# Kernel optimization log

Hardware: AMD Instinct MI355X
Metric: run time of the kernel (lower is better)

## Reference

```python
import jax, jax.numpy as jnp
import numpy as np

N = 100000        # nodes
E = 1600000       # directed edges (avg degree 16)
EMB = 32          # emb_hidden_dim
HID = 16          # hidden
Q = 0.25          # magnetic charge
NUM_SYMP = 15
BY = 4            # num_birthyear_disc


def _norm(edge_index, edge_weight):
    # Magnetic Laplacian, 'sym' normalization, lambda_max=2:
    # L_hat(u,v) = -deg^{-1/2}(u) * A_sym(u,v) * deg^{-1/2}(v) * exp(i*theta(u,v)),
    # theta = 2*pi*q*(A - A^T); diagonal of scaled L_hat is 0.
    src, dst = edge_index[0], edge_index[1]
    src2 = jnp.concatenate([src, dst])
    dst2 = jnp.concatenate([dst, src])
    sym_w = jnp.concatenate([edge_weight, edge_weight]) * 0.5
    theta = (2.0 * jnp.pi * Q) * jnp.concatenate([edge_weight, -edge_weight])
    deg = jax.ops.segment_sum(sym_w, dst2, num_segments=N)
    dinv = jnp.where(deg > 0, jax.lax.rsqrt(jnp.where(deg > 0, deg, 1.0)), 0.0)
    norm = dinv[src2] * sym_w * dinv[dst2]
    return src2, dst2, -norm * jnp.cos(theta), -norm * jnp.sin(theta)


def _cmatvec(src2, dst2, a_re, a_im, xr, xi):
    # complex sparse matvec: (A_re + i A_im)(x_re + i x_im)
    xr_s, xi_s = xr[src2], xi[src2]
    yr = jax.ops.segment_sum(a_re[:, None] * xr_s - a_im[:, None] * xi_s, dst2, num_segments=N)
    yi = jax.ops.segment_sum(a_re[:, None] * xi_s + a_im[:, None] * xr_s, dst2, num_segments=N)
    return yr, yi


def _magnet_conv(xr, xi, adj, W, b):
    # Chebyshev recursion T0=x, T1=L_hat x, T2=2 L_hat T1 - T0; out = sum_k T_k @ W[k] + b
    src2, dst2, a_re, a_im = adj
    out_r = xr @ W[0]
    out_i = xi @ W[0]
    t1r, t1i = _cmatvec(src2, dst2, a_re, a_im, xr, xi)
    out_r = out_r + t1r @ W[1]
    out_i = out_i + t1i @ W[1]
    t2r, t2i = _cmatvec(src2, dst2, a_re, a_im, t1r, t1i)
    t2r = 2.0 * t2r - xr
    t2i = 2.0 * t2i - xi
    out_r = out_r + t2r @ W[2]
    out_i = out_i + t2i @ W[2]
    return out_r + b, out_i + b


def setup_inputs() -> dict:
    key = jax.random.key(0)
    ks = jax.random.split(key, 12)
    birth = jax.random.randint(ks[0], (N,), 0, BY)
    gender = jax.random.randint(ks[1], (N,), 0, 2)
    symp = jax.random.randint(ks[2], (N, NUM_SYMP), 0, 3)
    x = jnp.concatenate([
        jax.nn.one_hot(birth, BY, dtype=jnp.int32),
        gender[:, None].astype(jnp.int32),
        symp.astype(jnp.int32),
    ], axis=1)  # [N, 20]
    edge_index = jax.random.randint(ks[3], (2, E), 0, N)
    edge_weight = jnp.ones((E,), jnp.float32)
    s = 0.1
    return {
        'x': x,
        'edge_index': edge_index,
        'edge_weight': edge_weight,
        'birth_tab': jax.random.normal(ks[4], (BY, EMB), jnp.float32) * s,
        'gender_tab': jax.random.normal(ks[5], (2, EMB), jnp.float32) * s,
        'symp_tab': jax.random.normal(ks[6], (NUM_SYMP, 3, EMB), jnp.float32) * s,
        'W1': jax.random.normal(ks[7], (3, EMB, HID), jnp.float32) * s,
        'b1': jnp.zeros((HID,), jnp.float32),
        'W2': jax.random.normal(ks[8], (3, HID, HID), jnp.float32) * s,
        'b2': jnp.zeros((HID,), jnp.float32),
        'Wc': jax.random.normal(ks[9], (2 * HID, 2 * HID), jnp.float32) * s,  # Conv1d k=1 (out,in)
        'bc': jnp.zeros((2 * HID,), jnp.float32),
        'Wl': jax.random.normal(ks[10], (2 * HID, 1), jnp.float32) * s,
        'bl': jnp.zeros((1,), jnp.float32),
    }


def reference(x, edge_index, edge_weight, birth_tab, gender_tab, symp_tab,
              W1, b1, W2, b2, Wc, bc, Wl, bl):
    # embedding gathers + mean fusion
    birth_idx = jnp.argmax(x[:, :BY] == 1, axis=1)
    birth_e = birth_tab[birth_idx]                              # [N, EMB]
    gender_e = gender_tab[x[:, BY]]                             # [N, EMB]
    symp_e = symp_tab[jnp.arange(NUM_SYMP)[None, :], x[:, -NUM_SYMP:]]  # [N, 15, EMB]
    feat = jnp.mean(symp_e, axis=1)
    h = (birth_e + gender_e + feat) / 3.0                       # [N, EMB]
    # complex Chebyshev spectral graph conv layers
    adj = _norm(edge_index, edge_weight)
    re, im = _magnet_conv(h, h, adj, W1, b1)
    re, im = _magnet_conv(re, im, adj, W2, b2)
    z = jnp.concatenate([re, im], axis=-1)                      # [N, 2*HID]
    z = z @ Wc.T + bc                                           # Conv1d kernel_size=1
    y = z @ Wl + bl                                             # Linear(2*HID, 1)
    return y[:, 0]
```

## Files before the change

### kernel.cpp

```cpp
#include <hip/hip_runtime.h>
#include <hip/hip_fp16.h>
#include <math.h>

static constexpr float PI2Q = 1.57079632679489662f;
#define NRANGE 8
#define NS2 16
#define MAXRNG 13056

__device__ __forceinline__ float2 h2f_bits(int b) {
  __half2 h = *reinterpret_cast<__half2*>(&b);
  return __half22float2(h);
}
__device__ __forceinline__ int f2h_bits(float a, float b) {
  __half2 h = __floats2half2_rn(a, b);
  return *reinterpret_cast<int*>(&h);
}

__global__ void k_weff(const float* __restrict__ Wc, const float* __restrict__ bc,
                       const float* __restrict__ Wl, const float* __restrict__ bl,
                       float* __restrict__ weff) {
  int k = threadIdx.x;
  if (k < 32) {
    float s = 0.f;
    #pragma unroll
    for (int j = 0; j < 32; ++j) s += Wc[j * 32 + k] * Wl[j];
    weff[k] = s;
  } else if (k == 32) {
    float s = 0.f;
    for (int j = 0; j < 32; ++j) s += bc[j] * Wl[j];
    weff[32] = s + bl[0];
  }
}

__global__ __launch_bounds__(256) void k_embed(
    const int* __restrict__ x, const float* __restrict__ btab,
    const float* __restrict__ gtab, const float* __restrict__ stab,
    const float* __restrict__ W1, const float* __restrict__ b1,
    float* __restrict__ PQ, __half2* __restrict__ PQh, float* __restrict__ o0, int n) {
  __shared__ float sm[3184];
  int tid = threadIdx.x;
  for (int t = tid; t < 1536; t += 256) sm[t] = W1[t];
  if (tid < 16) sm[1536 + tid] = b1[tid];
  for (int t = tid; t < 128; t += 256) sm[1552 + t] = btab[t];
  for (int t = tid; t < 64; t += 256) sm[1680 + t] = gtab[t];
  for (int t = tid; t < 1440; t += 256) sm[1744 + t] = stab[t];
  __syncthreads();
  int i = blockIdx.x * 256 + tid;
  if (i >= n) return;
  int xr[20];
  #pragma unroll
  for (int j = 0; j < 20; ++j) xr[j] = x[i * 20 + j];
  int bi = 0;
  #pragma unroll
  for (int j = 3; j >= 0; --j) if (xr[j] == 1) bi = j;
  int g = xr[4];
  float h[32];
  #pragma unroll
  for (int f = 0; f < 32; ++f) {
    float s = 0.f;
    #pragma unroll
    for (int j = 0; j < 15; ++j) s += sm[1744 + j * 96 + xr[5 + j] * 32 + f];
    h[f] = (sm[1552 + bi * 32 + f] + sm[1680 + g * 32 + f] + s * (1.f / 15.f)) * (1.f / 3.f);
  }
  #pragma unroll
  for (int f = 0; f < 16; ++f) {
    float o = sm[1536 + f], p = 0.f, q = 0.f;
    #pragma unroll
    for (int k = 0; k < 32; ++k) {
      float hk = h[k];
      o = fmaf(hk, sm[k * 16 + f], o);
      p = fmaf(hk, sm[512 + k * 16 + f], p);
      q = fmaf(hk, sm[1024 + k * 16 + f], q);
    }
    o0[i * 16 + f] = o;
    PQ[i * 32 + 2 * f] = p;
    PQ[i * 32 + 2 * f + 1] = q;
    PQh[(size_t)i * 16 + f] = __floats2half2_rn(p, q);
  }
}

__global__ __launch_bounds__(256) void k_rhist(const int* __restrict__ ei, int* __restrict__ rcnt,
                                               int rng, int E_) {
  __shared__ int h[8 * 16];
  int tid = threadIdx.x;
  if (tid < 128) h[tid] = 0;
  __syncthreads();
  int slot = tid & 15;
  int stride = gridDim.x * 256;
  for (int e = blockIdx.x * 256 + tid; e < E_; e += stride) {
    int s = ei[e], d = ei[E_ + e];
    atomicAdd(&h[(d / rng) * 16 + slot], 1);
    atomicAdd(&h[(s / rng) * 16 + slot], 1);
  }
  __syncthreads();
  if (tid < 8) {
    int sum = 0;
    #pragma unroll
    for (int j = 0; j < 16; ++j) sum += h[tid * 16 + j];
    atomicAdd(&rcnt[tid], sum);
  }
}

__global__ void k_rbase(const int* __restrict__ rcnt, int* __restrict__ rbase, int* __restrict__ rcur) {
  if (threadIdx.x == 0) {
    int run = 0;
    for (int r = 0; r < NRANGE; ++r) { rbase[r] = run; rcur[r] = run; run += rcnt[r]; }
    rbase[NRANGE] = run;
  }
}

__global__ __launch_bounds__(256) void k_bucket(const int* __restrict__ ei, const float* __restrict__ ew,
                                                int* __restrict__ rcur, int* __restrict__ brow,
                                                int2* __restrict__ bsw, int rng, int E_) {
  __shared__ int lcnt[NRANGE];
  __shared__ int gbase[NRANGE];
  int tid = threadIdx.x;
  if (tid < NRANGE) lcnt[tid] = 0;
  __syncthreads();
  int e0 = blockIdx.x * 1024;
  int s[4], d[4], wb[4], ra[4], rb[4], la[4], lb[4];
  #pragma unroll
  for (int j = 0; j < 4; ++j) {
    int e = e0 + j * 256 + tid;
    if (e < E_) {
      s[j] = ei[e]; d[j] = ei[E_ + e]; wb[j] = __float_as_int(ew[e]);
      ra[j] = d[j] / rng; rb[j] = s[j] / rng;
      la[j] = atomicAdd(&lcnt[ra[j]], 1);
      lb[j] = atomicAdd(&lcnt[rb[j]], 1);
    } else {
      ra[j] = -1; rb[j] = -1; s[j] = 0; d[j] = 0; wb[j] = 0; la[j] = 0; lb[j] = 0;
    }
  }
  __syncthreads();
  if (tid < NRANGE) gbase[tid] = lcnt[tid] ? atomicAdd(&rcur[tid], lcnt[tid]) : 0;
  __syncthreads();
  #pragma unroll
  for (int j = 0; j < 4; ++j) {
    if (ra[j] >= 0) {
      int pA = gbase[ra[j]] + la[j];
      brow[pA] = d[j];
      bsw[pA] = make_int2(s[j], wb[j]);
      int pB = gbase[rb[j]] + lb[j];
      brow[pB] = s[j];
      bsw[pB] = make_int2(d[j] | (int)0x80000000, wb[j]);
    }
  }
}

__global__ __launch_bounds__(1024) void k_hist2(const int* __restrict__ brow, const int* __restrict__ rbase,
                                                int* __restrict__ Hg, int rng) {
  __shared__ int hist[MAXRNG];
  int r = blockIdx.x & (NRANGE - 1);
  int st = blockIdx.x >> 3;
  int tid = threadIdx.x;
  for (int t = tid; t < rng; t += 1024) hist[t] = 0;
  __syncthreads();
  int b0 = rbase[r], bcnt = rbase[r + 1] - b0;
  int sl = (bcnt + NS2 - 1) / NS2;
  int k0 = b0 + st * sl, k1 = min(b0 + bcnt, k0 + sl);
  int base = r * rng;
  for (int k = k0 + tid; k < k1; k += 1024)
    atomicAdd(&hist[brow[k] - base], 1);
  __syncthreads();
  int* plane = Hg + (size_t)(r * NS2 + st) * rng;
  for (int t = tid; t < rng; t += 1024) plane[t] = hist[t];
}

__global__ __launch_bounds__(512) void k_scanH(int* __restrict__ Hg, int* __restrict__ cnt,
                                               int rng, int n) {
  int v = blockIdx.x * 512 + threadIdx.x;
  if (v >= n) return;
  int r = v / rng;
  int vloc = v - r * rng;
  int run = 0;
  size_t idx = (size_t)(r * NS2) * rng + vloc;
  #pragma unroll 4
  for (int s = 0; s < NS2; ++s) {
    int t = Hg[idx];
    Hg[idx] = run;
    run += t;
    idx += rng;
  }
  cnt[v] = run;
}

__global__ __launch_bounds__(1024) void k_scan_a(const int* __restrict__ cnt, int* __restrict__ rowp,
                                                 int* __restrict__ bsum, int n) {
  __shared__ int sh[1024];
  int tid = threadIdx.x;
  int idx = blockIdx.x * 1024 + tid;
  int v = (idx < n) ? cnt[idx] : 0;
  sh[tid] = v;
  __syncthreads();
  for (int offd = 1; offd < 1024; offd <<= 1) {
    int t = (tid >= offd) ? sh[tid - offd] : 0;
    __syncthreads();
    sh[tid] += t;
    __syncthreads();
  }
  if (idx < n) rowp[idx] = sh[tid] - v;
  if (tid == 1023) bsum[blockIdx.x] = sh[1023];
}

__global__ __launch_bounds__(128) void k_scan_b(int* __restrict__ bsum, int nb,
                                                int* __restrict__ rowp, int n) {
  __shared__ int sh[128];
  int tid = threadIdx.x;
  int v = (tid < nb) ? bsum[tid] : 0;
  sh[tid] = v;
  __syncthreads();
  for (int offd = 1; offd < 128; offd <<= 1) {
    int t = (tid >= offd) ? sh[tid - offd] : 0;
    __syncthreads();
    sh[tid] += t;
    __syncthreads();
  }
  if (tid < nb) bsum[tid] = sh[tid] - v;
  if (tid == 127) rowp[n] = sh[127];
}

__global__ __launch_bounds__(1024) void k_scan_c(int* __restrict__ rowp, const int* __restrict__ bsum, int n) {
  int idx = blockIdx.x * 1024 + threadIdx.x;
  if (idx < n && blockIdx.x > 0) rowp[idx] += bsum[blockIdx.x];
}

__global__ __launch_bounds__(1024) void k_place2(const int* __restrict__ brow, const int2* __restrict__ bsw,
                                                 const int* __restrict__ rbase, const int* __restrict__ rowp,
                                                 const int* __restrict__ Hoff, int2* __restrict__ recs,
                                                 int rng) {
  __shared__ int hist[MAXRNG];
  int r = blockIdx.x & (NRANGE - 1);
  int st = blockIdx.x >> 3;
  int tid = threadIdx.x;
  for (int t = tid; t < rng; t += 1024) hist[t] = 0;
  __syncthreads();
  int b0 = rbase[r], bcnt = rbase[r + 1] - b0;
  int sl = (bcnt + NS2 - 1) / NS2;
  int k0 = b0 + st * sl, k1 = min(b0 + bcnt, k0 + sl);
  int base = r * rng;
  const int* plane = Hoff + (size_t)(r * NS2 + st) * rng;
  for (int k = k0 + tid; k < k1; k += 1024) {
    int row = brow[k];
    int rowloc = row - base;
    int lr = atomicAdd(&hist[rowloc], 1);
    recs[rowp[row] + plane[rowloc] + lr] = bsw[k];
  }
}

__global__ __launch_bounds__(256) void k_rowdeg(const int* __restrict__ rowp, const int2* __restrict__ recs,
                                                float* __restrict__ dinv, int n) {
  int wid = (blockIdx.x * 256 + threadIdx.x) >> 6;
  if (wid >= n) return;
  int lane = threadIdx.x & 63;
  int rs = rowp[wid], re = rowp[wid + 1];
  float sum = 0.f;
  for (int k = rs + lane; k < re; k += 64) sum += __int_as_float(recs[k].y);
  sum += __shfl_xor(sum, 1); sum += __shfl_xor(sum, 2);
  sum += __shfl_xor(sum, 4); sum += __shfl_xor(sum, 8);
  sum += __shfl_xor(sum, 16); sum += __shfl_xor(sum, 32);
  if (lane == 0) {
    float dg = 0.5f * sum;
    dinv[wid] = (dg > 0.f) ? rsqrtf(dg) : 0.f;
  }
}

__global__ __launch_bounds__(256) void k_norm(const int* __restrict__ rowp, int2* __restrict__ recs,
                                              const float* __restrict__ dinv, int n) {
  int wid = (blockIdx.x * 256 + threadIdx.x) >> 6;
  if (wid >= n) return;
  int lane = threadIdx.x & 63;
  float di = dinv[wid];
  int rs = rowp[wid], re = rowp[wid + 1];
  for (int k = rs + lane; k < re; k += 64) {
    int2 r = recs[k];
    int s = r.x & 0x7fffffff;
    float w = __int_as_float(r.y);
    float nrm = di * 0.5f * w * dinv[s];
    float sn, cs;
    sincosf(PI2Q * w, &sn, &cs);
    float ar = -nrm * cs;
    float ai = (r.x < 0) ? nrm * sn : -nrm * sn;
    recs[k].y = f2h_bits(ar, ai);
  }
}

__global__ __launch_bounds__(256, 8) void k_hop_sym(
    const int* __restrict__ rowp, const int2* __restrict__ recs,
    const __half2* __restrict__ PQh, __half2* __restrict__ Uh, float* __restrict__ AB, int n) {
  int wid = (blockIdx.x * 256 + threadIdx.x) >> 6;
  if (wid >= n) return;
  int lane = threadIdx.x & 63;
  int fq = lane & 3, su = lane >> 2;
  int rs = rowp[wid], rend = rowp[wid + 1];
  float aA[4] = {0.f, 0.f, 0.f, 0.f}, aB[4] = {0.f, 0.f, 0.f, 0.f};
  float aC[4] = {0.f, 0.f, 0.f, 0.f}, aD[4] = {0.f, 0.f, 0.f, 0.f};
  const long long* rq = reinterpret_cast<const long long*>(recs);
  const int4* Pq = reinterpret_cast<const int4*>(PQh);
  for (int k = rs + su; k < rend; k += 16) {
    long long r0 = __builtin_nontemporal_load(rq + k);
    int s = ((int)r0) & 0x7fffffff;
    float2 a = h2f_bits((int)(r0 >> 32));
    float wm = a.x - a.y, wp = a.x + a.y;
    int4 v = Pq[(size_t)s * 4 + fq];
    float2 x0 = h2f_bits(v.x), x1 = h2f_bits(v.y), x2 = h2f_bits(v.z), x3 = h2f_bits(v.w);
    aA[0] = fmaf(wm, x0.x, aA[0]); aB[0] = fmaf(wp, x0.x, aB[0]);
    aC[0] = fmaf(wm, x0.y, aC[0]); aD[0] = fmaf(wp, x0.y, aD[0]);
    aA[1] = fmaf(wm, x1.x, aA[1]); aB[1] = fmaf(wp, x1.x, aB[1]);
    aC[1] = fmaf(wm, x1.y, aC[1]); aD[1] = fmaf(wp, x1.y, aD[1]);
    aA[2] = fmaf(wm, x2.x, aA[2]); aB[2] = fmaf(wp, x2.x, aB[2]);
    aC[2] = fmaf(wm, x2.y, aC[2]); aD[2] = fmaf(wp, x2.y, aD[2]);
    aA[3] = fmaf(wm, x3.x, aA[3]); aB[3] = fmaf(wp, x3.x, aB[3]);
    aC[3] = fmaf(wm, x3.y, aC[3]); aD[3] = fmaf(wp, x3.y, aD[3]);
  }
  #pragma unroll
  for (int j = 0; j < 4; ++j) {
    aA[j] += __shfl_xor(aA[j], 4); aA[j] += __shfl_xor(aA[j], 8);
    aA[j] += __shfl_xor(aA[j], 16); aA[j] += __shfl_xor(aA[j], 32);
    aB[j] += __shfl_xor(aB[j], 4); aB[j] += __shfl_xor(aB[j], 8);
    aB[j] += __shfl_xor(aB[j], 16); aB[j] += __shfl_xor(aB[j], 32);
    aC[j] += __shfl_xor(aC[j], 4); aC[j] += __shfl_xor(aC[j], 8);
    aC[j] += __shfl_xor(aC[j], 16); aC[j] += __shfl_xor(aC[j], 32);
    aD[j] += __shfl_xor(aD[j], 4); aD[j] += __shfl_xor(aD[j], 8);
    aD[j] += __shfl_xor(aD[j], 16); aD[j] += __shfl_xor(aD[j], 32);
  }
  if (lane < 4) {
    *reinterpret_cast<float4*>(AB + wid * 32 + 8 * fq) = make_float4(aA[0], aB[0], aA[1], aB[1]);
    *reinterpret_cast<float4*>(AB + wid * 32 + 8 * fq + 4) = make_float4(aA[2], aB[2], aA[3], aB[3]);
    int4 hv;
    hv.x = f2h_bits(aC[0], aD[0]); hv.y = f2h_bits(aC[1], aD[1]);
    hv.z = f2h_bits(aC[2], aD[2]); hv.w = f2h_bits(aC[3], aD[3]);
    *reinterpret_cast<int4*>(Uh + (size_t)wid * 16 + 4 * fq) = hv;
  }
}

template <int MODE>
__global__ __launch_bounds__(256, 8) void k_hop_full(
    const int* __restrict__ rowp, const int2* __restrict__ recs,
    const __half2* __restrict__ Xh, float* __restrict__ Y, __half2* __restrict__ Yh,
    const float* __restrict__ o0, const float* __restrict__ AB, const float* __restrict__ PQ,
    const float* __restrict__ D, const float* __restrict__ weff, int n) {
  int wid = (blockIdx.x * 256 + threadIdx.x) >> 6;
  if (wid >= n) return;
  int lane = threadIdx.x & 63;
  int fq = lane & 3, su = lane >> 2;
  int rs = rowp[wid], rend = rowp[wid + 1];
  float aR[4] = {0.f, 0.f, 0.f, 0.f}, aI[4] = {0.f, 0.f, 0.f, 0.f};
  const long long* rq = reinterpret_cast<const long long*>(recs);
  const int4* Xq = reinterpret_cast<const int4*>(Xh);
  for (int k = rs + su; k < rend; k += 16) {
    long long r0 = __builtin_nontemporal_load(rq + k);
    int s = ((int)r0) & 0x7fffffff;
    float2 a = h2f_bits((int)(r0 >> 32));
    int4 v = Xq[(size_t)s * 4 + fq];
    float2 x0 = h2f_bits(v.x), x1 = h2f_bits(v.y), x2 = h2f_bits(v.z), x3 = h2f_bits(v.w);
    aR[0] = fmaf(a.x, x0.x, aR[0]); aR[0] = fmaf(-a.y, x0.y, aR[0]);
    aI[0] = fmaf(a.x, x0.y, aI[0]); aI[0] = fmaf(a.y, x0.x, aI[0]);
    aR[1] = fmaf(a.x, x1.x, aR[1]); aR[1] = fmaf(-a.y, x1.y, aR[1]);
    aI[1] = fmaf(a.x, x1.y, aI[1]); aI[1] = fmaf(a.y, x1.x, aI[1]);
    aR[2] = fmaf(a.x, x2.x, aR[2]); aR[2] = fmaf(-a.y, x2.y, aR[2]);
    aI[2] = fmaf(a.x, x2.y, aI[2]); aI[2] = fmaf(a.y, x2.x, aI[2]);
    aR[3] = fmaf(a.x, x3.x, aR[3]); aR[3] = fmaf(-a.y, x3.y, aR[3]);
    aI[3] = fmaf(a.x, x3.y, aI[3]); aI[3] = fmaf(a.y, x3.x, aI[3]);
  }
  #pragma unroll
  for (int j = 0; j < 4; ++j) {
    aR[j] += __shfl_xor(aR[j], 4); aR[j] += __shfl_xor(aR[j], 8);
    aR[j] += __shfl_xor(aR[j], 16); aR[j] += __shfl_xor(aR[j], 32);
    aI[j] += __shfl_xor(aI[j], 4); aI[j] += __shfl_xor(aI[j], 8);
    aI[j] += __shfl_xor(aI[j], 16); aI[j] += __shfl_xor(aI[j], 32);
  }
  if (MODE == 2) {
    float c = 0.f;
    if (lane < 4) {
      float4 d0 = *reinterpret_cast<const float4*>(D + wid * 32 + 8 * fq);
      float4 d1 = *reinterpret_cast<const float4*>(D + wid * 32 + 8 * fq + 4);
      float4 w0 = *reinterpret_cast<const float4*>(weff + 4 * fq);
      float4 w1 = *reinterpret_cast<const float4*>(weff + 16 + 4 * fq);
      c  = (d0.x + 2.f * aR[0]) * w0.x + (d0.y + 2.f * aI[0]) * w1.x;
      c += (d0.z + 2.f * aR[1]) * w0.y + (d0.w + 2.f * aI[1]) * w1.y;
      c += (d1.x + 2.f * aR[2]) * w0.z + (d1.y + 2.f * aI[2]) * w1.z;
      c += (d1.z + 2.f * aR[3]) * w0.w + (d1.w + 2.f * aI[3]) * w1.w;
    }
    c += __shfl_xor(c, 1); c += __shfl_xor(c, 2);
    if (lane == 0) Y[wid] = c + weff[32];
  } else if (lane < 4) {
    if (MODE == 0) {
      *reinterpret_cast<float4*>(Y + wid * 32 + 8 * fq) = make_float4(aR[0], aI[0], aR[1], aI[1]);
      *reinterpret_cast<float4*>(Y + wid * 32 + 8 * fq + 4) = make_float4(aR[2], aI[2], aR[3], aI[3]);
    } else {
      float4 o = *reinterpret_cast<const float4*>(o0 + wid * 16 + 4 * fq);
      float4 ab0 = *reinterpret_cast<const float4*>(AB + wid * 32 + 8 * fq);
      float4 ab1 = *reinterpret_cast<const float4*>(AB + wid * 32 + 8 * fq + 4);
      float4 pq0 = *reinterpret_cast<const float4*>(PQ + wid * 32 + 8 * fq);
      float4 pq1 = *reinterpret_cast<const float4*>(PQ + wid * 32 + 8 * fq + 4);
      float zr0 = o.x + ab0.x + 2.f * aR[0] - pq0.y;
      float zi0 = o.x + ab0.y + 2.f * aI[0] - pq0.y;
      float zr1 = o.y + ab0.z + 2.f * aR[1] - pq0.w;
      float zi1 = o.y + ab0.w + 2.f * aI[1] - pq0.w;
      float zr2 = o.z + ab1.x + 2.f * aR[2] - pq1.y;
      float zi2 = o.z + ab1.y + 2.f * aI[2] - pq1.y;
      float zr3 = o.w + ab1.z + 2.f * aR[3] - pq1.w;
      float zi3 = o.w + ab1.w + 2.f * aI[3] - pq1.w;
      *reinterpret_cast<float4*>(Y + wid * 32 + 8 * fq) = make_float4(zr0, zi0, zr1, zi1);
      *reinterpret_cast<float4*>(Y + wid * 32 + 8 * fq + 4) = make_float4(zr2, zi2, zr3, zi3);
      int4 hv;
      hv.x = f2h_bits(zr0, zi0); hv.y = f2h_bits(zr1, zi1);
      hv.z = f2h_bits(zr2, zi2); hv.w = f2h_bits(zr3, zi3);
      *reinterpret_cast<int4*>(Yh + (size_t)wid * 16 + 4 * fq) = hv;
    }
  }
}

__global__ __launch_bounds__(256) void k_d2(const float* __restrict__ X2, const float* __restrict__ T1,
                                            const float* __restrict__ W2g, const float* __restrict__ b2g,
                                            __half2* __restrict__ U2h, float* __restrict__ D, int n) {
  __shared__ float sm[1040];
  int tid = threadIdx.x;
  for (int t = tid; t < 768; t += 256) sm[t] = W2g[t];
  if (tid < 16) sm[768 + tid] = b2g[tid];
  __syncthreads();
  if (tid < 256) sm[784 + tid] = sm[tid] - sm[512 + tid];
  __syncthreads();
  int i = blockIdx.x * 256 + tid;
  if (i >= n) return;
  float re[16], im[16], tr[16], ti[16];
  #pragma unroll
  for (int k = 0; k < 16; ++k) {
    float2 a = *reinterpret_cast<const float2*>(X2 + i * 32 + 2 * k);
    re[k] = a.x; im[k] = a.y;
    float2 b = *reinterpret_cast<const float2*>(T1 + i * 32 + 2 * k);
    tr[k] = b.x; ti[k] = b.y;
  }
  #pragma unroll
  for (int f = 0; f < 16; ++f) {
    float ur = 0.f, ui = 0.f;
    float dr = sm[768 + f], di = sm[768 + f];
    #pragma unroll
    for (int k = 0; k < 16; ++k) {
      float w2 = sm[512 + k * 16 + f];
      float w1 = sm[256 + k * 16 + f];
      float w02 = sm[784 + k * 16 + f];
      ur = fmaf(tr[k], w2, ur);
      ui = fmaf(ti[k], w2, ui);
      dr = fmaf(re[k], w02, dr); dr = fmaf(tr[k], w1, dr);
      di = fmaf(im[k], w02, di); di = fmaf(ti[k], w1, di);
    }
    U2h[(size_t)i * 16 + f] = __floats2half2_rn(ur, ui);
    *reinterpret_cast<float2*>(D + i * 32 + 2 * f) = make_float2(dr, di);
  }
}

extern "C" void kernel_launch(void* const* d_in, const int* in_sizes, int n_in,
                              void* d_out, int out_size, void* d_ws, size_t ws_size,
                              hipStream_t stream) {
  const int* x = (const int*)d_in[0];
  const int* ei = (const int*)d_in[1];
  const float* ew = (const float*)d_in[2];
  const float* btab = (const float*)d_in[3];
  const float* gtab = (const float*)d_in[4];
  const float* stab = (const float*)d_in[5];
  const float* W1 = (const float*)d_in[6];
  const float* b1 = (const float*)d_in[7];
  const float* W2 = (const float*)d_in[8];
  const float* b2 = (const float*)d_in[9];
  const float* Wc = (const float*)d_in[10];
  const float* bc = (const float*)d_in[11];
  const float* Wl = (const float*)d_in[12];
  const float* bl = (const float*)d_in[13];
  float* yout = (float*)d_out;

  const int N_ = in_sizes[0] / 20;
  const int E_ = in_sizes[1] / 2;
  const int M_ = 2 * E_;
  const int rng = (N_ + NRANGE - 1) / NRANGE;

  size_t off = 0;
  auto take = [&](size_t bytes) -> void* {
    void* p = (char*)d_ws + off;
    off += (bytes + 255) & ~(size_t)255;
    return p;
  };
  float* PQ   = (float*)take((size_t)N_ * 32 * 4);
  float* o0   = (float*)take((size_t)N_ * 16 * 4);
  float* Ubuf = (float*)take((size_t)N_ * 32 * 4);
  float* ABuf = (float*)take((size_t)N_ * 32 * 4);
  float* X2   = (float*)take((size_t)N_ * 32 * 4);
  float* dinv = (float*)take((size_t)N_ * 4);
  int* cnt    = (int*)take((size_t)N_ * 4);
  int* rowp   = (int*)take((size_t)(N_ + 1) * 4);
  int* bsum   = (int*)take(1024 * 4);
  float* weff = (float*)take(64 * 4);
  int* rcnt   = (int*)take(NRANGE * 4);
  int* rbase  = (int*)take((NRANGE + 1) * 4);
  int* rcur   = (int*)take(NRANGE * 4);
  int* brow   = (int*)take((size_t)M_ * 4);
  int2* bsw   = (int2*)take((size_t)M_ * 8);
  int2* recs  = (int2*)take((size_t)M_ * 8);
  (void)ws_size; (void)n_in; (void)out_size;

  int* Hg      = (int*)PQ;
  __half2* PQh = (__half2*)brow;
  __half2* Uh  = (__half2*)((char*)brow + (size_t)N_ * 64);
  __half2* X2h = (__half2*)bsw;
  __half2* U2h = (__half2*)((char*)bsw + (size_t)N_ * 64);

  int nbN = (N_ + 255) / 256;
  int nbS = (N_ + 1023) / 1024;
  int nbH = (N_ + 3) / 4;
  int nbT = (N_ + 511) / 512;
  int nbB = (E_ + 1023) / 1024;

  hipMemsetAsync(rcnt, 0, NRANGE * 4, stream);

  k_weff<<<1, 64, 0, stream>>>(Wc, bc, Wl, bl, weff);

  k_rhist<<<512, 256, 0, stream>>>(ei, rcnt, rng, E_);
  k_rbase<<<1, 64, 0, stream>>>(rcnt, rbase, rcur);
  k_bucket<<<nbB, 256, 0, stream>>>(ei, ew, rcur, brow, bsw, rng, E_);
  k_hist2<<<NRANGE * NS2, 1024, 0, stream>>>(brow, rbase, Hg, rng);
  k_scanH<<<nbT, 512, 0, stream>>>(Hg, cnt, rng, N_);
  k_scan_a<<<nbS, 1024, 0, stream>>>(cnt, rowp, bsum, N_);
  k_scan_b<<<1, 128, 0, stream>>>(bsum, nbS, rowp, N_);
  k_scan_c<<<nbS, 1024, 0, stream>>>(rowp, bsum, N_);
  k_place2<<<NRANGE * NS2, 1024, 0, stream>>>(brow, bsw, rbase, rowp, Hg, recs, rng);

  k_embed<<<nbN, 256, 0, stream>>>(x, btab, gtab, stab, W1, b1, PQ, PQh, o0, N_);
  k_rowdeg<<<nbH, 256, 0, stream>>>(rowp, recs, dinv, N_);
  k_norm<<<nbH, 256, 0, stream>>>(rowp, recs, dinv, N_);

  k_hop_sym<<<nbH, 256, 0, stream>>>(rowp, recs, PQh, Uh, ABuf, N_);
  k_hop_full<1><<<nbH, 256, 0, stream>>>(rowp, recs, Uh, X2, X2h, o0, ABuf, PQ,
                                         nullptr, nullptr, N_);
  k_hop_full<0><<<nbH, 256, 0, stream>>>(rowp, recs, X2h, Ubuf, nullptr, nullptr,
                                         nullptr, nullptr, nullptr, nullptr, N_);
  k_d2<<<nbN, 256, 0, stream>>>(X2, Ubuf, W2, b2, U2h, ABuf, N_);
  k_hop_full<2><<<nbH, 256, 0, stream>>>(rowp, recs, U2h, yout, nullptr, nullptr,
                                         nullptr, nullptr, ABuf, weff, N_);
}
```

Baseline: 495.9 us.

## Bucket edges by (row range, source group) key so CSR records are column-sorted

```diff
diff --git a/kernel.cpp b/kernel.cpp
--- a/kernel.cpp
+++ b/kernel.cpp
@@ -5,6 +5,8 @@
 static constexpr float PI2Q = 1.57079632679489662f;
 #define NRANGE 8
 #define NS2 16
+#define GSH2 13
+#define NKEY (NRANGE * NS2)
 #define MAXRNG 13056
 
 __device__ __forceinline__ float2 h2f_bits(int b) {
@@ -14,6 +16,10 @@
 __device__ __forceinline__ int f2h_bits(float a, float b) {
   __half2 h = __floats2half2_rn(a, b);
   return *reinterpret_cast<int*>(&h);
+}
+__device__ __forceinline__ int grp_of(int s) {
+  int g = s >> GSH2;
+  return (g > NS2 - 1) ? (NS2 - 1) : g;
 }
 
 __global__ void k_weff(const float* __restrict__ Wc, const float* __restrict__ bc,
@@ -81,66 +87,69 @@
 
 __global__ __launch_bounds__(256) void k_rhist(const int* __restrict__ ei, int* __restrict__ rcnt,
                                                int rng, int E_) {
-  __shared__ int h[8 * 16];
-  int tid = threadIdx.x;
-  if (tid < 128) h[tid] = 0;
-  __syncthreads();
-  int slot = tid & 15;
+  __shared__ int h[NKEY * 8];
+  int tid = threadIdx.x;
+  for (int t = tid; t < NKEY * 8; t += 256) h[t] = 0;
+  __syncthreads();
+  int slot = tid & 7;
   int stride = gridDim.x * 256;
   for (int e = blockIdx.x * 256 + tid; e < E_; e += stride) {
     int s = ei[e], d = ei[E_ + e];
-    atomicAdd(&h[(d / rng) * 16 + slot], 1);
-    atomicAdd(&h[(s / rng) * 16 + slot], 1);
-  }
-  __syncthreads();
-  if (tid < 8) {
+    int keyA = ((d / rng) << 4) | grp_of(s);
+    int keyB = ((s / rng) << 4) | grp_of(d);
+    atomicAdd(&h[keyA * 8 + slot], 1);
+    atomicAdd(&h[keyB * 8 + slot], 1);
+  }
+  __syncthreads();
+  for (int t = tid; t < NKEY; t += 256) {
     int sum = 0;
     #pragma unroll
-    for (int j = 0; j < 16; ++j) sum += h[tid * 16 + j];
-    atomicAdd(&rcnt[tid], sum);
+    for (int j = 0; j < 8; ++j) sum += h[t * 8 + j];
+    if (sum) atomicAdd(&rcnt[t], sum);
   }
 }
 
 __global__ void k_rbase(const int* __restrict__ rcnt, int* __restrict__ rbase, int* __restrict__ rcur) {
   if (threadIdx.x == 0) {
     int run = 0;
-    for (int r = 0; r < NRANGE; ++r) { rbase[r] = run; rcur[r] = run; run += rcnt[r]; }
-    rbase[NRANGE] = run;
+    for (int r = 0; r < NKEY; ++r) { rbase[r] = run; rcur[r] = run; run += rcnt[r]; }
+    rbase[NKEY] = run;
   }
 }
 
 __global__ __launch_bounds__(256) void k_bucket(const int* __restrict__ ei, const float* __restrict__ ew,
                                                 int* __restrict__ rcur, int* __restrict__ brow,
                                                 int2* __restrict__ bsw, int rng, int E_) {
-  __shared__ int lcnt[NRANGE];
-  __shared__ int gbase[NRANGE];
-  int tid = threadIdx.x;
-  if (tid < NRANGE) lcnt[tid] = 0;
+  __shared__ int lcnt[NKEY];
+  __shared__ int gbase[NKEY];
+  int tid = threadIdx.x;
+  if (tid < NKEY) lcnt[tid] = 0;
   __syncthreads();
   int e0 = blockIdx.x * 1024;
-  int s[4], d[4], wb[4], ra[4], rb[4], la[4], lb[4];
+  int s[4], d[4], wb[4], kA[4], kB[4], la[4], lb[4];
   #pragma unroll
   for (int j = 0; j < 4; ++j) {
     int e = e0 + j * 256 + tid;
     if (e < E_) {
       s[j] = ei[e]; d[j] = ei[E_ + e]; wb[j] = __float_as_int(ew[e]);
-      ra[j] = d[j] / rng; rb[j] = s[j] / rng;
-      la[j] = atomicAdd(&lcnt[ra[j]], 1);
-      lb[j] = atomicAdd(&lcnt[rb[j]], 1);
+      kA[j] = ((d[j] / rng) << 4) | grp_of(s[j]);
+      kB[j] = ((s[j] / rng) << 4) | grp_of(d[j]);
+      la[j] = atomicAdd(&lcnt[kA[j]], 1);
+      lb[j] = atomicAdd(&lcnt[kB[j]], 1);
     } else {
-      ra[j] = -1; rb[j] = -1; s[j] = 0; d[j] = 0; wb[j] = 0; la[j] = 0; lb[j] = 0;
+      kA[j] = -1; kB[j] = -1; s[j] = 0; d[j] = 0; wb[j] = 0; la[j] = 0; lb[j] = 0;
     }
   }
   __syncthreads();
-  if (tid < NRANGE) gbase[tid] = lcnt[tid] ? atomicAdd(&rcur[tid], lcnt[tid]) : 0;
+  if (tid < NKEY) gbase[tid] = lcnt[tid] ? atomicAdd(&rcur[tid], lcnt[tid]) : 0;
   __syncthreads();
   #pragma unroll
   for (int j = 0; j < 4; ++j) {
-    if (ra[j] >= 0) {
-      int pA = gbase[ra[j]] + la[j];
+    if (kA[j] >= 0) {
+      int pA = gbase[kA[j]] + la[j];
       brow[pA] = d[j];
       bsw[pA] = make_int2(s[j], wb[j]);
-      int pB = gbase[rb[j]] + lb[j];
+      int pB = gbase[kB[j]] + lb[j];
       brow[pB] = s[j];
       bsw[pB] = make_int2(d[j] | (int)0x80000000, wb[j]);
     }
@@ -152,12 +161,11 @@
   __shared__ int hist[MAXRNG];
   int r = blockIdx.x & (NRANGE - 1);
   int st = blockIdx.x >> 3;
+  int key = (r << 4) | st;
   int tid = threadIdx.x;
   for (int t = tid; t < rng; t += 1024) hist[t] = 0;
   __syncthreads();
-  int b0 = rbase[r], bcnt = rbase[r + 1] - b0;
-  int sl = (bcnt + NS2 - 1) / NS2;
-  int k0 = b0 + st * sl, k1 = min(b0 + bcnt, k0 + sl);
+  int k0 = rbase[key], k1 = rbase[key + 1];
   int base = r * rng;
   for (int k = k0 + tid; k < k1; k += 1024)
     atomicAdd(&hist[brow[k] - base], 1);
@@ -231,12 +239,11 @@
   __shared__ int hist[MAXRNG];
   int r = blockIdx.x & (NRANGE - 1);
   int st = blockIdx.x >> 3;
+  int key = (r << 4) | st;
   int tid = threadIdx.x;
   for (int t = tid; t < rng; t += 1024) hist[t] = 0;
   __syncthreads();
-  int b0 = rbase[r], bcnt = rbase[r + 1] - b0;
-  int sl = (bcnt + NS2 - 1) / NS2;
-  int k0 = b0 + st * sl, k1 = min(b0 + bcnt, k0 + sl);
+  int k0 = rbase[key], k1 = rbase[key + 1];
   int base = r * rng;
   const int* plane = Hoff + (size_t)(r * NS2 + st) * rng;
   for (int k = k0 + tid; k < k1; k += 1024) {
@@ -490,9 +497,9 @@
   int* rowp   = (int*)take((size_t)(N_ + 1) * 4);
   int* bsum   = (int*)take(1024 * 4);
   float* weff = (float*)take(64 * 4);
-  int* rcnt   = (int*)take(NRANGE * 4);
-  int* rbase  = (int*)take((NRANGE + 1) * 4);
-  int* rcur   = (int*)take(NRANGE * 4);
+  int* rcnt   = (int*)take(NKEY * 4);
+  int* rbase  = (int*)take((NKEY + 1) * 4);
+  int* rcur   = (int*)take(NKEY * 4);
   int* brow   = (int*)take((size_t)M_ * 4);
   int2* bsw   = (int2*)take((size_t)M_ * 8);
   int2* recs  = (int2*)take((size_t)M_ * 8);
@@ -510,7 +517,7 @@
   int nbT = (N_ + 511) / 512;
   int nbB = (E_ + 1023) / 1024;
 
-  hipMemsetAsync(rcnt, 0, NRANGE * 4, stream);
+  hipMemsetAsync(rcnt, 0, NKEY * 4, stream);
 
   k_weff<<<1, 64, 0, stream>>>(Wc, bc, Wl, bl, weff);
 
```

Result: slower. 540.1 us (+8.9%).
